# Kernel tuning notes

Hardware: AMD Instinct MI355X
Metric: run time of the kernel (lower is better)

Reference implementation:

```python
import jax, jax.numpy as jnp
import numpy as np

B, H, T, D = 8, 8, 8192, 64
NC, WSZ = 128, 64
COMMITMENT = 1e-4
EPS = 1e-5  # scatter_mean eps from routing-transformer


def setup_inputs() -> dict:
    key = jax.random.key(0)
    kq, kk, kv, km = jax.random.split(key, 4)
    q = jax.random.normal(kq, (B, H, T, D), jnp.float32)
    k = jax.random.normal(kk, (B, H, T, D), jnp.float32)
    v = jax.random.normal(kv, (B, H, T, D), jnp.float32)
    means = jax.random.normal(km, (H, NC, D), jnp.float32)  # kmeans centroids
    return {"q": q, "k": k, "v": v, "means": means}


def _l2norm(x):
    # F.normalize(x, 2, dim=-1)
    return x / jnp.clip(jnp.linalg.norm(x, axis=-1, keepdims=True), 1e-12)


def reference(q, k, v, means):
    b, h, t, d = q.shape
    nc = means.shape[1]
    wsz = min(WSZ, t)

    # ---- Kmeans routing (non-shared-qk branch: cluster cat(q,k)) ----
    x = jnp.concatenate([q, k], axis=2)           # (b,h,2t,d)
    xn = _l2norm(x)
    dists = jnp.einsum('bhtd,hcd->bhtc', xn, means)   # cosine sims
    dists = jax.lax.stop_gradient(dists)              # torch computes under no_grad
    buckets = jnp.argmax(dists, axis=-1)              # (b,h,2t)
    routed = means[jnp.arange(h)[None, :, None], buckets]  # (b,h,2t,d)
    aux_loss = jnp.mean((xn - routed) ** 2) * COMMITMENT   # commitment mse loss

    q_dists, k_dists = dists[:, :, :t], dists[:, :, t:]

    def topk_idx(dd, w):
        # torch: dd.topk(k=w, dim=-2).indices.transpose(-2,-1) -> (b,h,nc,w), flattened
        _, idx = jax.lax.top_k(jnp.swapaxes(dd, -1, -2), w)  # (b,h,nc,w)
        return idx.reshape(b, h, nc * w)

    indices = topk_idx(q_dists, wsz)      # (b,h,nc*wsz)
    kv_indices = topk_idx(k_dists, wsz)

    # ---- gather routed q/k/v into clusters ----
    gather = lambda arr, idx: jnp.take_along_axis(arr, idx[..., None], axis=2)
    qg = gather(q, indices).reshape(b, h, nc, wsz, d)
    kg = gather(k, kv_indices).reshape(b, h, nc, wsz, d)
    vg = gather(v, kv_indices).reshape(b, h, nc, wsz, d)

    # ---- per-cluster attention ----
    dots = jnp.einsum('bhnid,bhnjd->bhnij', qg, kg) * (d ** -0.5)
    attn = jax.nn.softmax(dots, axis=-1)
    bo = jnp.einsum('bhnij,bhnjd->bhnid', attn, vg)
    so = bo.reshape(b, h, nc * wsz, d)

    # ---- scatter_mean back to token order ----
    def scat(s, i):  # s: (N,d), i: (N,)
        num = jnp.zeros((t, d), s.dtype).at[i].add(s)
        den = jnp.zeros((t, 1), s.dtype).at[i].add(jnp.ones((i.shape[0], 1), s.dtype))
        return num / (den + EPS)

    out = jax.vmap(jax.vmap(scat))(so, indices)  # (b,h,t,d)
    return out, aux_loss
```

## Files before the change

### kernel.cpp

```cpp
#include <hip/hip_runtime.h>
#include <hip/hip_bf16.h>
#include <hip/hip_fp16.h>
#include <math.h>

#define B_ 8
#define H_ 8
#define T_ 8192
#define D_ 64
#define NC_ 128
#define WSZ_ 64
#define T2_ (2*T_)
#define BH_ (B_*H_)
#define CAP_ 16
#define SA 72

#define OFF_AUX    0
#define OFF_DEN    4096
#define OFF_QIDX   (OFF_DEN  + BH_*T_*4)
#define OFF_KIDX   (OFF_QIDX + BH_*NC_*WSZ_*4)
#define OFF_MEANST (OFF_KIDX + BH_*NC_*WSZ_*4)
#define OFF_DISTS  (OFF_MEANST + H_*NC_*D_*4)
#define SO_BYTES      ((size_t)BH_*NC_*WSZ_*D_*2)
#define ENTRIES_BYTES ((size_t)BH_*T_*CAP_*4)

__device__ __forceinline__ float2 h2f(unsigned u) {
    __half2 h = *reinterpret_cast<__half2*>(&u);
    return __half22float2(h);
}
__device__ __forceinline__ unsigned f2h2(float a, float b) {
    __half2 h = __float22half2_rn(make_float2(a, b));
    return *reinterpret_cast<unsigned*>(&h);
}

__global__ __launch_bounds__(256)
void k_meanst(const float* __restrict__ means, float* __restrict__ meanst)
{
    int gid = blockIdx.x * 256 + threadIdx.x;
    int h = gid >> 13;
    int rem = gid & 8191;
    int d = rem >> 7;
    int c = rem & 127;
    meanst[gid] = means[((h << 7) | c) * 64 + d];
}

__global__ __launch_bounds__(256)
void k_dists(const float* __restrict__ q, const float* __restrict__ k,
             const float* __restrict__ means, const float* __restrict__ meanst,
             float* __restrict__ dists, float* __restrict__ aux, int bh_base)
{
    __shared__ float xs[64 * 68];
    __shared__ int   bcs[64];
    __shared__ float ar[4];

    const int tid = threadIdx.x;
    const int bhl = blockIdx.y;
    const int bh  = bh_base + bhl;
    const int h   = bh % H_;
    const int t0  = blockIdx.x * 64;

    const int lane = tid & 63;
    const int w    = tid >> 6;
    for (int it = 0; it < 16; ++it) {
        int tl = it * 4 + w;
        int gt = t0 + tl;
        const float* src = (gt < T_)
            ? (q + ((size_t)bh * T_ + gt) * D_)
            : (k + ((size_t)bh * T_ + (gt - T_)) * D_);
        float vv = __builtin_nontemporal_load(src + lane);
        float s = vv * vv;
        #pragma unroll
        for (int off = 32; off > 0; off >>= 1) s += __shfl_xor(s, off);
        float norm = fmaxf(sqrtf(s), 1e-12f);
        xs[lane * 68 + tl] = vv / norm;
    }
    __syncthreads();

    const int ty = tid >> 4;
    const int tx = tid & 15;
    float acc[4][8];
    #pragma unroll
    for (int i = 0; i < 4; ++i)
        #pragma unroll
        for (int j = 0; j < 8; ++j) acc[i][j] = 0.f;

    const float* mt = meanst + (size_t)h * (64 * 128) + tx * 8;
    #pragma unroll 4
    for (int d = 0; d < 64; ++d) {
        float4 ma = *(const float4*)(mt + d * 128);
        float4 mb = *(const float4*)(mt + d * 128 + 4);
        float4 xa = *(const float4*)&xs[d * 68 + ty * 4];
        float xv[4] = {xa.x, xa.y, xa.z, xa.w};
        float mv[8] = {ma.x, ma.y, ma.z, ma.w, mb.x, mb.y, mb.z, mb.w};
        #pragma unroll
        for (int i = 0; i < 4; ++i)
            #pragma unroll
            for (int j = 0; j < 8; ++j)
                acc[i][j] = fmaf(xv[i], mv[j], acc[i][j]);
    }

    #pragma unroll
    for (int j = 0; j < 8; ++j) {
        const int c = tx * 8 + j;
        float* gp = dists + ((size_t)(bhl * NC_ + c)) * T2_ + t0 + ty * 4;
        *(float4*)gp = make_float4(acc[0][j], acc[1][j], acc[2][j], acc[3][j]);
    }

    #pragma unroll
    for (int i = 0; i < 4; ++i) {
        float bv = -1e30f; int bcid = 0;
        #pragma unroll
        for (int j = 0; j < 8; ++j) {
            float vv = acc[i][j];
            if (vv > bv) { bv = vv; bcid = tx * 8 + j; }
        }
        #pragma unroll
        for (int off = 1; off < 16; off <<= 1) {
            float ov = __shfl_xor(bv, off);
            int   oc = __shfl_xor(bcid, off);
            if (ov > bv || (ov == bv && oc < bcid)) { bv = ov; bcid = oc; }
        }
        if (tx == 0) bcs[ty * 4 + i] = bcid;
    }
    __syncthreads();

    float part = 0.f;
    for (int it = 0; it < 16; ++it) {
        int tl = it * 4 + w;
        int cb = bcs[tl];
        const float* mr = means + ((size_t)(h * NC_ + cb)) * 64;
        float df = xs[lane * 68 + tl] - mr[lane];
        part = fmaf(df, df, part);
    }
    #pragma unroll
    for (int off = 32; off > 0; off >>= 1) part += __shfl_xor(part, off);
    if (lane == 0) ar[w] = part;
    __syncthreads();
    if (tid == 0) atomicAdd(aux, ar[0] + ar[1] + ar[2] + ar[3]);
}

__device__ __forceinline__ unsigned flip_f32(float f) {
    unsigned bits = __float_as_uint(f);
    return (bits & 0x80000000u) ? ~bits : (bits | 0x80000000u);
}

__global__ __launch_bounds__(256)
void k_topk(const float* __restrict__ dists, int* __restrict__ qidx,
            int* __restrict__ kidx, int bh_base)
{
    __shared__ unsigned hist[4096];
    __shared__ unsigned sfx[256];
    __shared__ unsigned wtot[4];
    __shared__ unsigned cand_u[768];
    __shared__ int      cand_i[768];
    __shared__ int sh[6];

    const int tid   = threadIdx.x;
    const int c     = blockIdx.x;
    const int bhl   = blockIdx.y;
    const int which = blockIdx.z;
    const float* row = dists + ((size_t)(bhl * NC_ + c)) * T2_ + (size_t)which * T_;
    int* outp = (which ? kidx : qidx) + ((size_t)((bh_base + bhl) * NC_ + c)) * WSZ_;

    unsigned u[32];
    {
        const float4* r4 = (const float4*)row;
        #pragma unroll
        for (int it = 0; it < 8; ++it) {
            float4 f = r4[it * 256 + tid];
            u[it * 4 + 0] = flip_f32(f.x);
            u[it * 4 + 1] = flip_f32(f.y);
            u[it * 4 + 2] = flip_f32(f.z);
            u[it * 4 + 3] = flip_f32(f.w);
        }
    }
    for (int i = tid; i < 4096; i += 256) hist[i] = 0;
    if (tid < 6) sh[tid] = (tid < 2) ? -1 : 0;
    __syncthreads();

    #pragma unroll
    for (int j = 0; j < 32; ++j) atomicAdd(&hist[u[j] >> 20], 1u);
    __syncthreads();

    unsigned gs = 0;
    #pragma unroll
    for (int j = 0; j < 16; ++j) gs += hist[tid * 16 + j];

    const int l = tid & 63, w = tid >> 6;
    unsigned sv = gs;
    #pragma unroll
    for (int off = 1; off < 64; off <<= 1) {
        unsigned up = __shfl_down(sv, off);
        if (l + off < 64) sv += up;
    }
    if (l == 0) wtot[w] = sv;
    __syncthreads();
    unsigned hi = 0;
    for (int ww = w + 1; ww < 4; ++ww) hi += wtot[ww];
    unsigned suffix = sv + hi;
    sfx[tid] = suffix;
    if (suffix >= WSZ_) atomicMax(&sh[0], tid);
    __syncthreads();
    const int g1 = sh[0];
    const unsigned above_groups = (g1 < 255) ? sfx[g1 + 1] : 0u;

    if (tid < 16) {
        unsigned bs = above_groups;
        for (int j = 15; j >= tid; --j) bs += hist[g1 * 16 + j];
        if (bs >= WSZ_) atomicMax(&sh[1], g1 * 16 + tid);
    }
    __syncthreads();
    const int b1 = sh[1];
    if (tid == 0) {
        unsigned gt = above_groups;
        for (int j = b1 + 1; j <= g1 * 16 + 15; ++j) gt += hist[j];
        sh[4] = WSZ_ - (int)gt;
    }
    __syncthreads();
    const int kk = sh[4];

    #pragma unroll
    for (int j = 0; j < 32; ++j) {
        int bin = (int)(u[j] >> 20);
        int idx = (j >> 2) * 1024 + tid * 4 + (j & 3);
        if (bin > b1) {
            int p = atomicAdd(&sh[2], 1);
            outp[p] = idx;
        } else if (bin == b1) {
            int p = atomicAdd(&sh[3], 1);
            if (p < 768) { cand_u[p] = u[j]; cand_i[p] = idx; }
        }
    }
    __syncthreads();
    const int G = sh[2];
    const int C = sh[3];

    if (C <= 768) {
        for (int j = tid; j < C; j += 256) {
            unsigned uj = cand_u[j]; int ij = cand_i[j];
            int rank = 0;
            for (int ll = 0; ll < C; ++ll) {
                unsigned ul = cand_u[ll];
                rank += (int)((ul > uj) || (ul == uj && cand_i[ll] < ij));
            }
            if (rank < kk) outp[G + rank] = ij;
        }
        return;
    }

    unsigned prefix = 0, mask = 0;
    int need = WSZ_;
    for (int shift = 24; shift >= 0; shift -= 8) {
        if (tid < 256) hist[tid] = 0;
        __syncthreads();
        for (int it = 0; it < 32; ++it) {
            unsigned uu = flip_f32(row[it * 256 + tid]);
            if ((uu & mask) == prefix) atomicAdd(&hist[(uu >> shift) & 255u], 1u);
        }
        __syncthreads();
        if (tid == 0) {
            int b = 255;
            int k2 = need;
            while (b > 0) {
                int cnt = (int)hist[b];
                if (k2 - cnt <= 0) break;
                k2 -= cnt; --b;
            }
            sh[0] = k2; sh[1] = b;
        }
        __syncthreads();
        need = sh[0];
        prefix |= ((unsigned)sh[1]) << shift;
        mask   |= 0xFFu << shift;
        __syncthreads();
    }
    if (tid == 0) { sh[2] = 0; sh[3] = 0; }
    __syncthreads();
    const unsigned thr = prefix;
    for (int it = 0; it < 32; ++it) {
        int i = it * 256 + tid;
        unsigned uu = flip_f32(row[i]);
        if (uu > thr) {
            int p = atomicAdd(&sh[2], 1);
            outp[p] = i;
        } else if (uu == thr) {
            int p = atomicAdd(&sh[3], 1);
            if (p < 768) cand_i[p] = i;
        }
    }
    __syncthreads();
    if (tid == 0) {
        int base = sh[2];
        int E = sh[3] < 768 ? sh[3] : 768;
        for (int n = 0; n < need; ++n) {
            int mi = 0x7fffffff, mj = 0;
            for (int j = 0; j < E; ++j) {
                int vv = cand_i[j];
                if (vv < mi) { mi = vv; mj = j; }
            }
            cand_i[mj] = 0x7fffffff;
            outp[base + n] = mi;
        }
    }
}

__global__ __launch_bounds__(256)
void k_attn_w(const float* __restrict__ q, const float* __restrict__ k,
              const float* __restrict__ v, const int* __restrict__ qidx,
              const int* __restrict__ kidx, unsigned* __restrict__ so,
              int* __restrict__ cnt, int* __restrict__ entries,
              float* __restrict__ out)
{
    __shared__ __half Ah[64 * SA];
    __shared__ __half Bh[64 * SA];
    __shared__ int qi[64], ki[64], lp[64];

    const int tid = threadIdx.x;
    const int c  = blockIdx.x;
    const int bh = blockIdx.y;
    const int* qp = qidx + ((size_t)(bh * NC_ + c)) * WSZ_;
    const int* kp = kidx + ((size_t)(bh * NC_ + c)) * WSZ_;
    if (tid < 64) { qi[tid] = qp[tid]; ki[tid] = kp[tid]; }
    __syncthreads();

    const int grow = tid >> 2, gseg = (tid & 3) * 16;
    {
        const float4* qsrc = (const float4*)(q + ((size_t)bh * T_ + qi[grow]) * D_ + gseg);
        const float4* ksrc = (const float4*)(k + ((size_t)bh * T_ + ki[grow]) * D_ + gseg);
        unsigned* qd = (unsigned*)&Ah[grow * SA + gseg];
        unsigned* kd = (unsigned*)&Bh[grow * SA + gseg];
        #pragma unroll
        for (int j4 = 0; j4 < 4; ++j4) {
            float4 fq = qsrc[j4];
            float4 fk = ksrc[j4];
            qd[j4 * 2 + 0] = f2h2(fq.x, fq.y);
            qd[j4 * 2 + 1] = f2h2(fq.z, fq.w);
            kd[j4 * 2 + 0] = f2h2(fk.x, fk.y);
            kd[j4 * 2 + 1] = f2h2(fk.z, fk.w);
        }
    }
    __syncthreads();

    const int tx = tid & 15;
    const int ty = tid >> 4;

    float sacc[4][4];
    #pragma unroll
    for (int i = 0; i < 4; ++i)
        #pragma unroll
        for (int j = 0; j < 4; ++j) sacc[i][j] = 0.f;

    for (int k4 = 0; k4 < 16; ++k4) {
        float2 qf[8];
        #pragma unroll
        for (int i = 0; i < 4; ++i) {
            uint2 qr = *(const uint2*)&Ah[(ty * 4 + i) * SA + k4 * 4];
            qf[i * 2 + 0] = h2f(qr.x);
            qf[i * 2 + 1] = h2f(qr.y);
        }
        #pragma unroll
        for (int j = 0; j < 4; ++j) {
            uint2 kr = *(const uint2*)&Bh[(tx + j * 16) * SA + k4 * 4];
            float2 k01 = h2f(kr.x), k23 = h2f(kr.y);
            #pragma unroll
            for (int i = 0; i < 4; ++i)
                sacc[i][j] = fmaf(qf[i*2+1].y, k23.y, fmaf(qf[i*2+1].x, k23.x,
                              fmaf(qf[i*2+0].y, k01.y, fmaf(qf[i*2+0].x, k01.x, sacc[i][j]))));
        }
    }
    __syncthreads();

    {
        const float4* vsrc = (const float4*)(v + ((size_t)bh * T_ + ki[grow]) * D_ + gseg);
        unsigned* vd = (unsigned*)&Bh[grow * SA + gseg];
        #pragma unroll
        for (int j4 = 0; j4 < 4; ++j4) {
            float4 f = vsrc[j4];
            vd[j4 * 2 + 0] = f2h2(f.x, f.y);
            vd[j4 * 2 + 1] = f2h2(f.z, f.w);
        }
    }

    if (tx == 0) {
        #pragma unroll
        for (int i = 0; i < 4; ++i) {
            int r = ty * 4 + i;
            int t = qi[r];
            int p = atomicAdd(&cnt[(size_t)bh * T_ + t], 1);
            if (p < CAP_) entries[((size_t)bh * T_ + t) * CAP_ + p] = c * WSZ_ + r;
            lp[r] = p;
        }
    }

    float rinv[4];
    #pragma unroll
    for (int i = 0; i < 4; ++i) {
        float m = fmaxf(fmaxf(sacc[i][0], sacc[i][1]), fmaxf(sacc[i][2], sacc[i][3]));
        m = fmaxf(m, __shfl_xor(m, 1));
        m = fmaxf(m, __shfl_xor(m, 2));
        m = fmaxf(m, __shfl_xor(m, 4));
        m = fmaxf(m, __shfl_xor(m, 8));
        float e0 = expf((sacc[i][0] - m) * 0.125f);
        float e1 = expf((sacc[i][1] - m) * 0.125f);
        float e2 = expf((sacc[i][2] - m) * 0.125f);
        float e3 = expf((sacc[i][3] - m) * 0.125f);
        float s = e0 + e1 + e2 + e3;
        s += __shfl_xor(s, 1);
        s += __shfl_xor(s, 2);
        s += __shfl_xor(s, 4);
        s += __shfl_xor(s, 8);
        rinv[i] = 1.0f / s;
        const int rb = (ty * 4 + i) * SA + tx;
        Ah[rb     ] = __float2half(e0);
        Ah[rb + 16] = __float2half(e1);
        Ah[rb + 32] = __float2half(e2);
        Ah[rb + 48] = __float2half(e3);
    }
    __syncthreads();

    float oacc[4][4];
    #pragma unroll
    for (int i = 0; i < 4; ++i)
        #pragma unroll
        for (int j = 0; j < 4; ++j) oacc[i][j] = 0.f;

    for (int jj4 = 0; jj4 < 16; ++jj4) {
        float2 v01[4], v23[4];
        #pragma unroll
        for (int ll = 0; ll < 4; ++ll) {
            uint2 r = *(const uint2*)&Bh[(jj4 * 4 + ll) * SA + tx * 4];
            v01[ll] = h2f(r.x);
            v23[ll] = h2f(r.y);
        }
        #pragma unroll
        for (int i = 0; i < 4; ++i) {
            uint2 pr = *(const uint2*)&Ah[(ty * 4 + i) * SA + jj4 * 4];
            float2 p01 = h2f(pr.x), p23 = h2f(pr.y);
            oacc[i][0] = fmaf(p23.y, v01[3].x, fmaf(p23.x, v01[2].x, fmaf(p01.y, v01[1].x, fmaf(p01.x, v01[0].x, oacc[i][0]))));
            oacc[i][1] = fmaf(p23.y, v01[3].y, fmaf(p23.x, v01[2].y, fmaf(p01.y, v01[1].y, fmaf(p01.x, v01[0].y, oacc[i][1]))));
            oacc[i][2] = fmaf(p23.y, v23[3].x, fmaf(p23.x, v23[2].x, fmaf(p01.y, v23[1].x, fmaf(p01.x, v23[0].x, oacc[i][2]))));
            oacc[i][3] = fmaf(p23.y, v23[3].y, fmaf(p23.x, v23[2].y, fmaf(p01.y, v23[1].y, fmaf(p01.x, v23[0].y, oacc[i][3]))));
        }
    }

    #pragma unroll
    for (int i = 0; i < 4; ++i) {
        const int r = ty * 4 + i;
        float o0 = oacc[i][0] * rinv[i];
        float o1 = oacc[i][1] * rinv[i];
        float o2 = oacc[i][2] * rinv[i];
        float o3 = oacc[i][3] * rinv[i];
        unsigned* dst = so + (((size_t)(bh * NC_ + c)) * WSZ_ + r) * (D_ / 2) + tx * 2;
        uint2 pk;
        pk.x = f2h2(o0, o1);
        pk.y = f2h2(o2, o3);
        *(uint2*)dst = pk;
        if (lp[r] >= CAP_) {
            float* ob = out + ((size_t)bh * T_ + qi[r]) * D_ + tx * 4;
            atomicAdd(ob + 0, o0); atomicAdd(ob + 1, o1);
            atomicAdd(ob + 2, o2); atomicAdd(ob + 3, o3);
        }
    }
}

__global__ __launch_bounds__(256)
void k_gather(const unsigned* __restrict__ so, const int* __restrict__ cnt,
              const int* __restrict__ entries, float* __restrict__ out,
              const float* __restrict__ aux)
{
    const int tid = threadIdx.x;
    const int tk  = blockIdx.x * 16 + (tid >> 4);
    const int bh  = blockIdx.y;
    const int d4  = (tid & 15) * 2;
    const size_t tix = (size_t)bh * T_ + tk;

    const int n = cnt[tix];
    const int m = n < CAP_ ? n : CAP_;
    const int* ep = entries + tix * CAP_;

    float a0 = 0.f, a1 = 0.f, a2 = 0.f, a3 = 0.f;
    for (int j = 0; j < m; ++j) {
        int e = ep[j];
        const unsigned* sp = so + ((size_t)bh * (NC_ * WSZ_) + e) * (D_ / 2) + d4;
        uint2 raw = *(const uint2*)sp;
        float2 f01 = h2f(raw.x), f23 = h2f(raw.y);
        a0 += f01.x; a1 += f01.y; a2 += f23.x; a3 += f23.y;
    }
    float* op = out + tix * D_ + (tid & 15) * 4;
    float4 pr = *(float4*)op;
    float inv = 1.0f / ((float)n + 1e-5f);
    float4 r;
    r.x = (a0 + pr.x) * inv;
    r.y = (a1 + pr.y) * inv;
    r.z = (a2 + pr.z) * inv;
    r.w = (a3 + pr.w) * inv;
    *(float4*)op = r;

    if (blockIdx.x == 0 && bh == 0 && tid == 0)
        out[(size_t)BH_ * T_ * D_] = aux[0] * 1.4901161193847656e-12f;
}

__global__ __launch_bounds__(256)
void k_attn(const float* __restrict__ q, const float* __restrict__ k,
            const float* __restrict__ v, const int* __restrict__ qidx,
            const int* __restrict__ kidx, float* __restrict__ out,
            float* __restrict__ den)
{
    __shared__ __half Ah[64 * SA];
    __shared__ __half Bh[64 * SA];
    __shared__ int qi[64], ki[64];

    const int tid = threadIdx.x;
    const int c  = blockIdx.x;
    const int bh = blockIdx.y;
    const int* qp = qidx + ((size_t)(bh * NC_ + c)) * WSZ_;
    const int* kp = kidx + ((size_t)(bh * NC_ + c)) * WSZ_;
    if (tid < 64) { qi[tid] = qp[tid]; ki[tid] = kp[tid]; }
    __syncthreads();

    const int grow = tid >> 2, gseg = (tid & 3) * 16;
    {
        const float4* qsrc = (const float4*)(q + ((size_t)bh * T_ + qi[grow]) * D_ + gseg);
        const float4* ksrc = (const float4*)(k + ((size_t)bh * T_ + ki[grow]) * D_ + gseg);
        unsigned* qd = (unsigned*)&Ah[grow * SA + gseg];
        unsigned* kd = (unsigned*)&Bh[grow * SA + gseg];
        #pragma unroll
        for (int j4 = 0; j4 < 4; ++j4) {
            float4 fq = qsrc[j4];
            float4 fk = ksrc[j4];
            qd[j4 * 2 + 0] = f2h2(fq.x, fq.y);
            qd[j4 * 2 + 1] = f2h2(fq.z, fq.w);
            kd[j4 * 2 + 0] = f2h2(fk.x, fk.y);
            kd[j4 * 2 + 1] = f2h2(fk.z, fk.w);
        }
    }
    __syncthreads();

    const int tx = tid & 15;
    const int ty = tid >> 4;

    float sacc[4][4];
    #pragma unroll
    for (int i = 0; i < 4; ++i)
        #pragma unroll
        for (int j = 0; j < 4; ++j) sacc[i][j] = 0.f;

    for (int k4 = 0; k4 < 16; ++k4) {
        float2 qf[8];
        #pragma unroll
        for (int i = 0; i < 4; ++i) {
            uint2 qr = *(const uint2*)&Ah[(ty * 4 + i) * SA + k4 * 4];
            qf[i * 2 + 0] = h2f(qr.x);
            qf[i * 2 + 1] = h2f(qr.y);
        }
        #pragma unroll
        for (int j = 0; j < 4; ++j) {
            uint2 kr = *(const uint2*)&Bh[(tx + j * 16) * SA + k4 * 4];
            float2 k01 = h2f(kr.x), k23 = h2f(kr.y);
            #pragma unroll
            for (int i = 0; i < 4; ++i)
                sacc[i][j] = fmaf(qf[i*2+1].y, k23.y, fmaf(qf[i*2+1].x, k23.x,
                              fmaf(qf[i*2+0].y, k01.y, fmaf(qf[i*2+0].x, k01.x, sacc[i][j]))));
        }
    }
    __syncthreads();

    {
        const float4* vsrc = (const float4*)(v + ((size_t)bh * T_ + ki[grow]) * D_ + gseg);
        unsigned* vd = (unsigned*)&Bh[grow * SA + gseg];
        #pragma unroll
        for (int j4 = 0; j4 < 4; ++j4) {
            float4 f = vsrc[j4];
            vd[j4 * 2 + 0] = f2h2(f.x, f.y);
            vd[j4 * 2 + 1] = f2h2(f.z, f.w);
        }
    }

    float rinv[4];
    #pragma unroll
    for (int i = 0; i < 4; ++i) {
        float m = fmaxf(fmaxf(sacc[i][0], sacc[i][1]), fmaxf(sacc[i][2], sacc[i][3]));
        m = fmaxf(m, __shfl_xor(m, 1));
        m = fmaxf(m, __shfl_xor(m, 2));
        m = fmaxf(m, __shfl_xor(m, 4));
        m = fmaxf(m, __shfl_xor(m, 8));
        float e0 = expf((sacc[i][0] - m) * 0.125f);
        float e1 = expf((sacc[i][1] - m) * 0.125f);
        float e2 = expf((sacc[i][2] - m) * 0.125f);
        float e3 = expf((sacc[i][3] - m) * 0.125f);
        float s = e0 + e1 + e2 + e3;
        s += __shfl_xor(s, 1);
        s += __shfl_xor(s, 2);
        s += __shfl_xor(s, 4);
        s += __shfl_xor(s, 8);
        rinv[i] = 1.0f / s;
        const int rb = (ty * 4 + i) * SA + tx;
        Ah[rb     ] = __float2half(e0);
        Ah[rb + 16] = __float2half(e1);
        Ah[rb + 32] = __float2half(e2);
        Ah[rb + 48] = __float2half(e3);
    }
    __syncthreads();

    float oacc[4][4];
    #pragma unroll
    for (int i = 0; i < 4; ++i)
        #pragma unroll
        for (int j = 0; j < 4; ++j) oacc[i][j] = 0.f;

    for (int jj4 = 0; jj4 < 16; ++jj4) {
        float2 v01[4], v23[4];
        #pragma unroll
        for (int ll = 0; ll < 4; ++ll) {
            uint2 r = *(const uint2*)&Bh[(jj4 * 4 + ll) * SA + tx * 4];
            v01[ll] = h2f(r.x);
            v23[ll] = h2f(r.y);
        }
        #pragma unroll
        for (int i = 0; i < 4; ++i) {
            uint2 pr = *(const uint2*)&Ah[(ty * 4 + i) * SA + jj4 * 4];
            float2 p01 = h2f(pr.x), p23 = h2f(pr.y);
            oacc[i][0] = fmaf(p23.y, v01[3].x, fmaf(p23.x, v01[2].x, fmaf(p01.y, v01[1].x, fmaf(p01.x, v01[0].x, oacc[i][0]))));
            oacc[i][1] = fmaf(p23.y, v01[3].y, fmaf(p23.x, v01[2].y, fmaf(p01.y, v01[1].y, fmaf(p01.x, v01[0].y, oacc[i][1]))));
            oacc[i][2] = fmaf(p23.y, v23[3].x, fmaf(p23.x, v23[2].x, fmaf(p01.y, v23[1].x, fmaf(p01.x, v23[0].x, oacc[i][2]))));
            oacc[i][3] = fmaf(p23.y, v23[3].y, fmaf(p23.x, v23[2].y, fmaf(p01.y, v23[1].y, fmaf(p01.x, v23[0].y, oacc[i][3]))));
        }
    }

    #pragma unroll
    for (int i = 0; i < 4; ++i) {
        const int r = ty * 4 + i;
        float* obase = out + ((size_t)bh * T_ + qi[r]) * D_ + tx * 4;
        #pragma unroll
        for (int j = 0; j < 4; ++j) atomicAdd(obase + j, oacc[i][j] * rinv[i]);
    }
    if (tx == 0) {
        #pragma unroll
        for (int i = 0; i < 4; ++i) atomicAdd(den + (size_t)bh * T_ + qi[ty * 4 + i], 1.0f);
    }
}

__global__ __launch_bounds__(256)
void k_final(float* __restrict__ out, const float* __restrict__ den,
             const float* __restrict__ aux)
{
    size_t gid = (size_t)blockIdx.x * 256 + threadIdx.x;
    float4* o4 = (float4*)out;
    float d = den[gid >> 4] + 1e-5f;
    float4 x = o4[gid];
    x.x = x.x / d; x.y = x.y / d; x.z = x.z / d; x.w = x.w / d;
    o4[gid] = x;
    if (gid == 0) out[(size_t)BH_ * T_ * D_] = aux[0] * 1.4901161193847656e-12f;
}

extern "C" void kernel_launch(void* const* d_in, const int* in_sizes, int n_in,
                              void* d_out, int out_size, void* d_ws, size_t ws_size,
                              hipStream_t stream) {
    const float* q     = (const float*)d_in[0];
    const float* k     = (const float*)d_in[1];
    const float* v     = (const float*)d_in[2];
    const float* means = (const float*)d_in[3];
    float* out = (float*)d_out;
    char*  ws  = (char*)d_ws;
    float* aux    = (float*)(ws + OFF_AUX);
    float* den    = (float*)(ws + OFF_DEN);
    int*   qidx   = (int*)(ws + OFF_QIDX);
    int*   kidx   = (int*)(ws + OFF_KIDX);
    float* meanst = (float*)(ws + OFF_MEANST);
    float* dists  = (float*)(ws + OFF_DISTS);

    hipMemsetAsync(out, 0, (size_t)((size_t)BH_ * T_ * D_ + 1) * 4, stream);
    hipMemsetAsync(ws, 0, (size_t)OFF_QIDX, stream);

    k_meanst<<<256, 256, 0, stream>>>(means, meanst);

    size_t region = (ws_size > OFF_DISTS) ? ws_size - (size_t)OFF_DISTS : 0;
    size_t per_bh = (size_t)NC_ * T2_ * 4;
    int nbh = (int)(region / per_bh);
    nbh = nbh < 1 ? 1 : (nbh > BH_ ? BH_ : nbh);
    const bool sopath = region >= (SO_BYTES + ENTRIES_BYTES);

    for (int bh_base = 0; bh_base < BH_; bh_base += nbh) {
        int cur = BH_ - bh_base < nbh ? BH_ - bh_base : nbh;
        k_dists<<<dim3(T2_ / 64, cur), 256, 0, stream>>>(q, k, means, meanst, dists, aux, bh_base);
        k_topk <<<dim3(NC_, cur, 2),    256, 0, stream>>>(dists, qidx, kidx, bh_base);
    }

    if (sopath) {
        unsigned* so = (unsigned*)(ws + OFF_DISTS);
        int* entries = (int*)(ws + OFF_DISTS + SO_BYTES);
        k_attn_w<<<dim3(NC_, BH_), 256, 0, stream>>>(q, k, v, qidx, kidx,
                                                     so, (int*)den, entries, out);
        k_gather<<<dim3(T_ / 16, BH_), 256, 0, stream>>>(so, (int*)den, entries, out, aux);
    } else {
        k_attn<<<dim3(NC_, BH_), 256, 0, stream>>>(q, k, v, qidx, kidx, out, den);
        k_final<<<(BH_ * T_ * D_ / 4 + 255) / 256, 256, 0, stream>>>(out, den, aux);
    }
}
```

Before: 1.003 ms.

## Remap k_dists thread tiling so each wave owns 32 clusters with scalar centroid loads

Changes the distance kernel's register tiling. Each lane now handles one token and each wave handles 32 centroids, using a wave-uniform (readfirstlane) pointer so centroid rows can be fetched as scalar/broadcast loads. Shared memory padding goes from 68 to 65 to avoid bank conflicts on the new column access, and the argmax is reduced across waves through shared memory instead of shuffles. Dists stores become per-lane coalesced rows. The trade-off is higher register pressure from 32 accumulators and less x reuse per centroid load.

```diff
diff --git a/kernel.cpp b/kernel.cpp
--- a/kernel.cpp
+++ b/kernel.cpp
@@ -13,6 +13,7 @@
 #define BH_ (B_*H_)
 #define CAP_ 16
 #define SA 72
+#define SX 65
 
 #define OFF_AUX    0
 #define OFF_DEN    4096
@@ -48,7 +49,9 @@
              const float* __restrict__ means, const float* __restrict__ meanst,
              float* __restrict__ dists, float* __restrict__ aux, int bh_base)
 {
-    __shared__ float xs[64 * 68];
+    __shared__ float xs[64 * SX];
+    __shared__ float bvs[4][64];
+    __shared__ int   bis[4][64];
     __shared__ int   bcs[64];
     __shared__ float ar[4];
 
@@ -57,9 +60,9 @@
     const int bh  = bh_base + bhl;
     const int h   = bh % H_;
     const int t0  = blockIdx.x * 64;
-
     const int lane = tid & 63;
     const int w    = tid >> 6;
+
     for (int it = 0; it < 16; ++it) {
         int tl = it * 4 + w;
         int gt = t0 + tl;
@@ -71,55 +74,50 @@
         #pragma unroll
         for (int off = 32; off > 0; off >>= 1) s += __shfl_xor(s, off);
         float norm = fmaxf(sqrtf(s), 1e-12f);
-        xs[lane * 68 + tl] = vv / norm;
-    }
-    __syncthreads();
-
-    const int ty = tid >> 4;
-    const int tx = tid & 15;
-    float acc[4][8];
-    #pragma unroll
-    for (int i = 0; i < 4; ++i)
-        #pragma unroll
-        for (int j = 0; j < 8; ++j) acc[i][j] = 0.f;
-
-    const float* mt = meanst + (size_t)h * (64 * 128) + tx * 8;
-    #pragma unroll 4
+        xs[lane * SX + tl] = vv / norm;
+    }
+    __syncthreads();
+
+    const int wu = __builtin_amdgcn_readfirstlane(w);
+    const float* mw = meanst + (size_t)h * (64 * 128) + wu * 32;
+
+    float acc[32];
+    #pragma unroll
+    for (int j = 0; j < 32; ++j) acc[j] = 0.f;
+
+    #pragma unroll 2
     for (int d = 0; d < 64; ++d) {
-        float4 ma = *(const float4*)(mt + d * 128);
-        float4 mb = *(const float4*)(mt + d * 128 + 4);
-        float4 xa = *(const float4*)&xs[d * 68 + ty * 4];
-        float xv[4] = {xa.x, xa.y, xa.z, xa.w};
-        float mv[8] = {ma.x, ma.y, ma.z, ma.w, mb.x, mb.y, mb.z, mb.w};
-        #pragma unroll
-        for (int i = 0; i < 4; ++i)
-            #pragma unroll
-            for (int j = 0; j < 8; ++j)
-                acc[i][j] = fmaf(xv[i], mv[j], acc[i][j]);
-    }
-
-    #pragma unroll
-    for (int j = 0; j < 8; ++j) {
-        const int c = tx * 8 + j;
-        float* gp = dists + ((size_t)(bhl * NC_ + c)) * T2_ + t0 + ty * 4;
-        *(float4*)gp = make_float4(acc[0][j], acc[1][j], acc[2][j], acc[3][j]);
-    }
-
-    #pragma unroll
-    for (int i = 0; i < 4; ++i) {
-        float bv = -1e30f; int bcid = 0;
-        #pragma unroll
-        for (int j = 0; j < 8; ++j) {
-            float vv = acc[i][j];
-            if (vv > bv) { bv = vv; bcid = tx * 8 + j; }
-        }
-        #pragma unroll
-        for (int off = 1; off < 16; off <<= 1) {
-            float ov = __shfl_xor(bv, off);
-            int   oc = __shfl_xor(bcid, off);
-            if (ov > bv || (ov == bv && oc < bcid)) { bv = ov; bcid = oc; }
-        }
-        if (tx == 0) bcs[ty * 4 + i] = bcid;
+        float xv = xs[d * SX + lane];
+        const float* mrow = mw + d * 128;
+        #pragma unroll
+        for (int j = 0; j < 32; ++j)
+            acc[j] = fmaf(xv, mrow[j], acc[j]);
+    }
+
+    {
+        float* gb = dists + ((size_t)(bhl * NC_ + wu * 32)) * T2_ + t0 + lane;
+        #pragma unroll
+        for (int j = 0; j < 32; ++j)
+            gb[(size_t)j * T2_] = acc[j];
+    }
+
+    {
+        float bv = acc[0]; int bj = 0;
+        #pragma unroll
+        for (int j = 1; j < 32; ++j)
+            if (acc[j] > bv) { bv = acc[j]; bj = j; }
+        bvs[w][lane] = bv;
+        bis[w][lane] = wu * 32 + bj;
+    }
+    __syncthreads();
+    if (tid < 64) {
+        float b = bvs[0][tid]; int bi = bis[0][tid];
+        #pragma unroll
+        for (int ww = 1; ww < 4; ++ww) {
+            float ov = bvs[ww][tid];
+            if (ov > b) { b = ov; bi = bis[ww][tid]; }
+        }
+        bcs[tid] = bi;
     }
     __syncthreads();
 
@@ -128,7 +126,7 @@
         int tl = it * 4 + w;
         int cb = bcs[tl];
         const float* mr = means + ((size_t)(h * NC_ + cb)) * 64;
-        float df = xs[lane * 68 + tl] - mr[lane];
+        float df = xs[lane * SX + tl] - mr[lane];
         part = fmaf(df, df, part);
     }
     #pragma unroll
```

Result: faster. 844.4 us (-15.8%).
